# Performance work log

Hardware: AMD Instinct MI355X
Metric: run time of the kernel (lower is better)

Reference implementation:

```python
import jax, jax.numpy as jnp
import numpy as np

N = 4_194_304          # number of rays
DAMPING = 0.5          # LM(0.5)
MAX_DELTA = 1000.0     # clamp on LM step
N_ITER = 30            # no_grad warmup iterations
XMIN, XMAX, TAU = -1.0, 1.0, 1.0


def _surface_F(pts, c):
    # implicit parabolic rod: F(p) = x - c*(y^2 + z^2); pts: [N,3]
    return pts[..., 0] - c * (pts[..., 1] ** 2 + pts[..., 2] ** 2)


def _lm_delta(P, V, t, c):
    # Levenberg-Marquardt step for f(t) = F(P + t*V):
    # delta = f * f' / (f'^2 + damping), clamped to [-max_delta, max_delta]
    pts = P + t[:, None] * V                     # [N,3]
    f = _surface_F(pts, c)                       # [N]
    # f'(t) = gradF(pts) . V, gradF = (1, -2c*y, -2c*z)
    fp = V[:, 0] - 2.0 * c * (pts[:, 1] * V[:, 1] + pts[:, 2] * V[:, 2])
    delta = f * fp / (fp * fp + DAMPING)
    return jnp.clip(delta, -MAX_DELTA, MAX_DELTA)


def setup_inputs() -> dict:
    key = jax.random.key(0)
    k1, k2 = jax.random.split(key, 2)
    P = jax.random.normal(k1, (N, 3), jnp.float32) * 2.0
    V = jax.random.normal(k2, (N, 3), jnp.float32)
    V = V / jnp.linalg.norm(V, axis=-1, keepdims=True)
    a, b = 0.3, -0.2
    Rz = jnp.array([[np.cos(a), -np.sin(a), 0.0],
                    [np.sin(a),  np.cos(a), 0.0],
                    [0.0,        0.0,       1.0]], jnp.float32)
    Ry = jnp.array([[np.cos(b), 0.0, np.sin(b)],
                    [0.0,       1.0, 0.0],
                    [-np.sin(b), 0.0, np.cos(b)]], jnp.float32)
    R = Rz @ Ry                                  # rigid rotation [3,3]
    T = jnp.array([0.1, -0.2, 0.05], jnp.float32)
    c = jnp.float32(0.05)
    loss_in = jnp.float32(0.0)
    return {"P": P, "V": V, "R": R, "T": T, "c": c, "loss_in": loss_in}


def reference(P, V, R, T, c, loss_in):
    n = P.shape[0]
    # transform.inverse_points / inverse_vectors: R^T (p - T), R^T v
    P_local = (P - T) @ R                        # [N,3]
    V_local = V @ R                              # [N,3]

    # 30 no-grad LM iterations (torch.no_grad -> stop_gradient on inputs)
    Pl = jax.lax.stop_gradient(P_local)
    Vl = jax.lax.stop_gradient(V_local)
    cs = jax.lax.stop_gradient(c)

    def body(i, t):
        return t - _lm_delta(Pl, Vl, t, cs)

    t0 = jax.lax.fori_loop(0, N_ITER, body, jnp.zeros((n,), jnp.float32))

    # final differentiable LM step
    t = t0 - _lm_delta(P_local, V_local, t0, c)

    points_local = P_local + t[:, None] * V_local
    scale = jnp.mean(jnp.abs(jnp.array([XMIN, XMAX, TAU], jnp.float32)))
    F = _surface_F(points_local, c) / scale
    loss = loss_in + jnp.sum(F ** 2) / n
    return loss
```

## Files before the change

kernel.cpp:

```cpp
#include <hip/hip_runtime.h>


#define LM_ITERS 31
constexpr float DAMPING = 0.5f;

struct F3 { float x, y, z; };

__global__ __launch_bounds__(256) void rod_kernel(
    const float* __restrict__ P, const float* __restrict__ V,
    const float* __restrict__ Rm, const float* __restrict__ Tv,
    const float* __restrict__ c_ptr, double* __restrict__ ws, int n)
{
    const float c  = c_ptr[0];
    const float r00 = Rm[0], r01 = Rm[1], r02 = Rm[2];
    const float r10 = Rm[3], r11 = Rm[4], r12 = Rm[5];
    const float r20 = Rm[6], r21 = Rm[7], r22 = Rm[8];
    const float t0 = Tv[0], t1 = Tv[1], t2 = Tv[2];

    const int lane = threadIdx.x & 63;
    const int wave = threadIdx.x >> 6;
    const int wbase = (blockIdx.x * 4 + wave) * 512;

    const F3* __restrict__ P3 = (const F3*)P;
    const F3* __restrict__ V3 = (const F3*)V;

    float px[8], py[8], pz[8], qx[8], qy[8], qz[8];

    if (wbase + 512 <= n) {
        #pragma unroll
        for (int r = 0; r < 8; ++r) {
            const int ray = wbase + 64 * r + lane;
            const F3 p = P3[ray];
            px[r] = p.x; py[r] = p.y; pz[r] = p.z;
        }
        #pragma unroll
        for (int r = 0; r < 8; ++r) {
            const int ray = wbase + 64 * r + lane;
            const F3 v = V3[ray];
            qx[r] = v.x; qy[r] = v.y; qz[r] = v.z;
        }
    } else {
        #pragma unroll
        for (int r = 0; r < 8; ++r) {
            const int ray = wbase + 64 * r + lane;
            if (ray < n) {
                px[r] = P[3 * ray + 0]; py[r] = P[3 * ray + 1]; pz[r] = P[3 * ray + 2];
                qx[r] = V[3 * ray + 0]; qy[r] = V[3 * ray + 1]; qz[r] = V[3 * ray + 2];
            } else {
                px[r] = py[r] = pz[r] = 0.0f;
                qx[r] = qy[r] = qz[r] = 0.0f;
            }
        }
    }

    float nA[8], f[8], fp[8];
    #pragma unroll
    for (int r = 0; r < 8; ++r) {
        const float ax = px[r] - t0, ay = py[r] - t1, az = pz[r] - t2;
        const float plx = ax * r00 + ay * r10 + az * r20;
        const float ply = ax * r01 + ay * r11 + az * r21;
        const float plz = ax * r02 + ay * r12 + az * r22;
        const float vlx = qx[r] * r00 + qy[r] * r10 + qz[r] * r20;
        const float vly = qx[r] * r01 + qy[r] * r11 + qz[r] * r21;
        const float vlz = qx[r] * r02 + qy[r] * r12 + qz[r] * r22;
        nA[r] = c * (vly * vly + vlz * vlz);
        f[r]  = plx - c * (ply * ply + plz * plz);
        fp[r] = vlx - 2.0f * c * (ply * vly + plz * vlz);
    }

    #pragma unroll 1
    for (int it = 0; it < LM_ITERS; ++it) {
        #pragma unroll
        for (int r = 0; r < 8; ++r) {
            const float den = fmaf(fp[r], fp[r], DAMPING);
            const float rcp = __builtin_amdgcn_rcpf(den);
            const float d   = (f[r] * fp[r]) * rcp;
            const float tmp = fmaf(nA[r], d, fp[r]);
            f[r]  = fmaf(-d, tmp, f[r]);
            fp[r] = fmaf(nA[r], d, tmp);
        }
    }

    double acc = 0.0;
    #pragma unroll
    for (int r = 0; r < 8; ++r)
        if (wbase + 64 * r + lane < n) acc += (double)f[r] * (double)f[r];

    for (int off = 32; off > 0; off >>= 1)
        acc += __shfl_down(acc, off, 64);
    __shared__ double sacc[4];
    if (lane == 0) sacc[wave] = acc;
    __syncthreads();
    if (threadIdx.x == 0) {
        atomicAdd(ws, sacc[0] + sacc[1] + sacc[2] + sacc[3]);
    }
}

__global__ void rod_finalize(const double* __restrict__ ws,
                             const float* __restrict__ loss_in,
                             float* __restrict__ out, double inv_n)
{
    out[0] = (float)(ws[0] * inv_n + (double)loss_in[0]);
}

extern "C" void kernel_launch(void* const* d_in, const int* in_sizes, int n_in,
                              void* d_out, int out_size, void* d_ws, size_t ws_size,
                              hipStream_t stream) {
    const float* P       = (const float*)d_in[0];
    const float* V       = (const float*)d_in[1];
    const float* R       = (const float*)d_in[2];
    const float* T       = (const float*)d_in[3];
    const float* c       = (const float*)d_in[4];
    const float* loss_in = (const float*)d_in[5];

    const int n = in_sizes[0] / 3;

    hipMemsetAsync(d_ws, 0, sizeof(double), stream);

    const int threads = (n + 7) / 8;
    const int block   = 256;
    const int grid    = (threads + block - 1) / block;
    rod_kernel<<<grid, block, 0, stream>>>(P, V, R, T, c, (double*)d_ws, n);
    rod_finalize<<<1, 1, 0, stream>>>((const double*)d_ws, loss_in,
                                      (float*)d_out, 1.0 / (double)n);
}
```

Before: 137.6 us.

## Software-pipeline ray chunks so next loads overlap current LM iterations

Each wave now handles 1024 rays in four chunks of 256 and issues the global loads for the next chunk before running the 31 LM iterations on the current one. The goal is to hide memory latency behind the compute-bound iteration loop. The grid shrinks by half, so fewer waves are in flight. That could lower occupancy-based latency hiding, and the prefetched chunk adds register pressure.

```diff
diff --git a/kernel.cpp b/kernel.cpp
--- a/kernel.cpp
+++ b/kernel.cpp
@@ -5,6 +5,8 @@
 constexpr float DAMPING = 0.5f;
 
 struct F3 { float x, y, z; };
+
+struct Rays4 { float px[4], py[4], pz[4], vx[4], vy[4], vz[4]; };
 
 __global__ __launch_bounds__(256) void rod_kernel(
     const float* __restrict__ P, const float* __restrict__ V,
@@ -19,72 +21,101 @@
 
     const int lane = threadIdx.x & 63;
     const int wave = threadIdx.x >> 6;
-    const int wbase = (blockIdx.x * 4 + wave) * 512;
+    const int wbase = (blockIdx.x * 4 + wave) * 1024;
 
     const F3* __restrict__ P3 = (const F3*)P;
     const F3* __restrict__ V3 = (const F3*)V;
 
-    float px[8], py[8], pz[8], qx[8], qy[8], qz[8];
-
-    if (wbase + 512 <= n) {
-        #pragma unroll
-        for (int r = 0; r < 8; ++r) {
-            const int ray = wbase + 64 * r + lane;
-            const F3 p = P3[ray];
-            px[r] = p.x; py[r] = p.y; pz[r] = p.z;
-        }
-        #pragma unroll
-        for (int r = 0; r < 8; ++r) {
-            const int ray = wbase + 64 * r + lane;
-            const F3 v = V3[ray];
-            qx[r] = v.x; qy[r] = v.y; qz[r] = v.z;
-        }
-    } else {
-        #pragma unroll
-        for (int r = 0; r < 8; ++r) {
-            const int ray = wbase + 64 * r + lane;
-            if (ray < n) {
-                px[r] = P[3 * ray + 0]; py[r] = P[3 * ray + 1]; pz[r] = P[3 * ray + 2];
-                qx[r] = V[3 * ray + 0]; qy[r] = V[3 * ray + 1]; qz[r] = V[3 * ray + 2];
-            } else {
-                px[r] = py[r] = pz[r] = 0.0f;
-                qx[r] = qy[r] = qz[r] = 0.0f;
+    auto load4 = [&](int cbase) -> Rays4 {
+        Rays4 q;
+        if (cbase + 256 <= n) {
+            #pragma unroll
+            for (int r = 0; r < 4; ++r) {
+                const F3 p = P3[cbase + 64 * r + lane];
+                q.px[r] = p.x; q.py[r] = p.y; q.pz[r] = p.z;
+            }
+            #pragma unroll
+            for (int r = 0; r < 4; ++r) {
+                const F3 v = V3[cbase + 64 * r + lane];
+                q.vx[r] = v.x; q.vy[r] = v.y; q.vz[r] = v.z;
+            }
+        } else {
+            #pragma unroll
+            for (int r = 0; r < 4; ++r) {
+                const int ray = cbase + 64 * r + lane;
+                if (ray < n) {
+                    q.px[r] = P[3 * ray + 0]; q.py[r] = P[3 * ray + 1]; q.pz[r] = P[3 * ray + 2];
+                    q.vx[r] = V[3 * ray + 0]; q.vy[r] = V[3 * ray + 1]; q.vz[r] = V[3 * ray + 2];
+                } else {
+                    q.px[r] = q.py[r] = q.pz[r] = 0.0f;
+                    q.vx[r] = q.vy[r] = q.vz[r] = 0.0f;
+                }
             }
         }
-    }
+        return q;
+    };
 
-    float nA[8], f[8], fp[8];
-    #pragma unroll
-    for (int r = 0; r < 8; ++r) {
-        const float ax = px[r] - t0, ay = py[r] - t1, az = pz[r] - t2;
-        const float plx = ax * r00 + ay * r10 + az * r20;
-        const float ply = ax * r01 + ay * r11 + az * r21;
-        const float plz = ax * r02 + ay * r12 + az * r22;
-        const float vlx = qx[r] * r00 + qy[r] * r10 + qz[r] * r20;
-        const float vly = qx[r] * r01 + qy[r] * r11 + qz[r] * r21;
-        const float vlz = qx[r] * r02 + qy[r] * r12 + qz[r] * r22;
-        nA[r] = c * (vly * vly + vlz * vlz);
-        f[r]  = plx - c * (ply * ply + plz * plz);
-        fp[r] = vlx - 2.0f * c * (ply * vly + plz * vlz);
-    }
+    float nA[4], f[4], fp[4];
 
-    #pragma unroll 1
-    for (int it = 0; it < LM_ITERS; ++it) {
+    auto setup4 = [&](const Rays4& q) {
         #pragma unroll
-        for (int r = 0; r < 8; ++r) {
-            const float den = fmaf(fp[r], fp[r], DAMPING);
-            const float rcp = __builtin_amdgcn_rcpf(den);
-            const float d   = (f[r] * fp[r]) * rcp;
-            const float tmp = fmaf(nA[r], d, fp[r]);
-            f[r]  = fmaf(-d, tmp, f[r]);
-            fp[r] = fmaf(nA[r], d, tmp);
+        for (int r = 0; r < 4; ++r) {
+            const float ax = q.px[r] - t0, ay = q.py[r] - t1, az = q.pz[r] - t2;
+            const float plx = ax * r00 + ay * r10 + az * r20;
+            const float ply = ax * r01 + ay * r11 + az * r21;
+            const float plz = ax * r02 + ay * r12 + az * r22;
+            const float vlx = q.vx[r] * r00 + q.vy[r] * r10 + q.vz[r] * r20;
+            const float vly = q.vx[r] * r01 + q.vy[r] * r11 + q.vz[r] * r21;
+            const float vlz = q.vx[r] * r02 + q.vy[r] * r12 + q.vz[r] * r22;
+            nA[r] = c * (vly * vly + vlz * vlz);
+            f[r]  = plx - c * (ply * ply + plz * plz);
+            fp[r] = vlx - 2.0f * c * (ply * vly + plz * vlz);
         }
-    }
+    };
+
+    auto iterate = [&]() {
+        #pragma unroll 1
+        for (int it = 0; it < LM_ITERS; ++it) {
+            #pragma unroll
+            for (int r = 0; r < 4; ++r) {
+                const float den = fmaf(fp[r], fp[r], DAMPING);
+                const float rcp = __builtin_amdgcn_rcpf(den);
+                const float d   = (f[r] * fp[r]) * rcp;
+                const float tmp = fmaf(nA[r], d, fp[r]);
+                f[r]  = fmaf(-d, tmp, f[r]);
+                fp[r] = fmaf(nA[r], d, tmp);
+            }
+        }
+    };
 
     double acc = 0.0;
-    #pragma unroll
-    for (int r = 0; r < 8; ++r)
-        if (wbase + 64 * r + lane < n) acc += (double)f[r] * (double)f[r];
+    auto accum = [&](int cbase) {
+        #pragma unroll
+        for (int r = 0; r < 4; ++r)
+            if (cbase + 64 * r + lane < n) acc += (double)f[r] * (double)f[r];
+    };
+
+    const int c0 = wbase, c1 = wbase + 256, c2 = wbase + 512, c3 = wbase + 768;
+
+    Rays4 q0 = load4(c0);
+    setup4(q0);
+    Rays4 q1 = load4(c1);
+    iterate();
+    accum(c0);
+
+    setup4(q1);
+    Rays4 q2 = load4(c2);
+    iterate();
+    accum(c1);
+
+    setup4(q2);
+    Rays4 q3 = load4(c3);
+    iterate();
+    accum(c2);
+
+    setup4(q3);
+    iterate();
+    accum(c3);
 
     for (int off = 32; off > 0; off >>= 1)
         acc += __shfl_down(acc, off, 64);
@@ -117,7 +148,7 @@
 
     hipMemsetAsync(d_ws, 0, sizeof(double), stream);
 
-    const int threads = (n + 7) / 8;
+    const int threads = (n + 15) / 16;
     const int block   = 256;
     const int grid    = (threads + block - 1) / block;
     rod_kernel<<<grid, block, 0, stream>>>(P, V, R, T, c, (double*)d_ws, n);
```

After: 149.5 us. 8.7% more time.
